# Optimization experiments

Measured on AMD Instinct MI355X. Metric: run time of the kernel, lower is better.

Reference implementation:

```python
import jax, jax.numpy as jnp
import numpy as np


def setup_inputs() -> dict:
    key = jax.random.key(0)
    k1, k2, k3, k4 = jax.random.split(key, 4)
    B, C, H, W = 4, 256, 64, 64
    Va = jax.random.normal(k1, (B, C, H, W), jnp.float32)
    Vb = jax.random.normal(k2, (B, C, H, W), jnp.float32)
    # nn.Linear(C, C, bias=False) weight, used as x @ W^T
    W_linear = jax.random.normal(k3, (C, C), jnp.float32) * 0.05
    # nn.Conv2d(C, 1, 1, bias=False) weight, init normal_(0, 0.01)
    W_gate = jax.random.normal(k4, (C,), jnp.float32) * 0.01
    return {"Va_output": Va, "Vb_output": Vb, "W_linear": W_linear,
            "W_gate": W_gate, "input_size": 512}


def reference(Va_output, Vb_output, W_linear, W_gate, input_size):
    B, C, H, W = Vb_output.shape
    A = H * W  # all_dim
    Va_flat = Va_output.reshape(B, C, A)  # [B, C, A]
    Vb_flat = Vb_output.reshape(B, C, A)
    # linear on transposed A-major tokens: Va_t @ W_linear^T -> [B, A, C]
    Va_corr = jnp.einsum('bca,dc->bad', Va_flat, W_linear)
    # correlation matrix S = Va_corr @ Vb_flat -> [B, A, A]
    S = jnp.einsum('bac,can->ban'[:3] + 'c,c' if False else 'bac,cn', Va_corr, Vb_flat) if False else jnp.einsum('bac,bcn->ban', Va_corr, Vb_flat)
    # S_c = softmax(S, dim=1); S_r = softmax(S^T, dim=1) = softmax(S, axis=2)^T
    S_c = jax.nn.softmax(S, axis=1)
    S_r = jnp.swapaxes(jax.nn.softmax(S, axis=2), 1, 2)
    Vb_att = jnp.einsum('bca,ban->bcn', Va_flat, S_r).reshape(B, C, H, W)
    Va_att = jnp.einsum('bca,ban->bcn', Vb_flat, S_c).reshape(B, C, H, W)
    # 1x1 gate conv (C -> 1, no bias) + sigmoid
    Va_mask = jax.nn.sigmoid(jnp.einsum('bchw,c->bhw', Va_att, W_gate))[:, None]
    Vb_mask = jax.nn.sigmoid(jnp.einsum('bchw,c->bhw', Vb_att, W_gate))[:, None]
    Va_out = jnp.concatenate([Va_att * Va_mask, Va_output], axis=1)  # [B, 2C, H, W]
    Vb_out = jnp.concatenate([Vb_att * Vb_mask, Vb_output], axis=1)
    return (Va_out, Vb_out, input_size)
```

## Files before the change

### kernel.cpp

```cpp
#include <hip/hip_runtime.h>

typedef _Float16 f16;
typedef f16 f16x8 __attribute__((ext_vector_type(8)));
typedef float f32x4 __attribute__((ext_vector_type(4)));
typedef short b16x8 __attribute__((ext_vector_type(8)));
typedef unsigned short u16;
typedef u16 u16x4 __attribute__((ext_vector_type(4)));

#define MFMA_F16(a,b,c)  __builtin_amdgcn_mfma_f32_16x16x32_f16((a),(b),(c),0,0,0)
#define MFMA_BF16(a,b,c) __builtin_amdgcn_mfma_f32_16x16x32_bf16((a),(b),(c),0,0,0)

static __device__ __forceinline__ u16 bf16rn(float f) {
    unsigned u = __builtin_bit_cast(unsigned, f);
    u += 0x7FFFu + ((u >> 16) & 1u);
    return (u16)(u >> 16);
}

typedef const __attribute__((address_space(1))) unsigned int* gas_p;
typedef __attribute__((address_space(3))) unsigned int* las_p;
static __device__ __forceinline__ void gll16(const void* g, void* l) {
    __builtin_amdgcn_global_load_lds((gas_p)g, (las_p)l, 16, 0, 0);
}

static constexpr int B_ = 4, C_ = 256, A_ = 4096;
static constexpr int CA   = C_ * A_;
static constexpr int BCA  = B_ * CA;
static constexpr int OUT_T = B_ * 2 * CA;
static constexpr size_t WS_Va16 = 0;
static constexpr size_t WS_Vb16 = WS_Va16 + (size_t)BCA;
static constexpr size_t WS_VaT  = WS_Vb16 + (size_t)BCA;
static constexpr size_t WS_VbT  = WS_VaT  + (size_t)BCA;
static constexpr size_t WS_Q1   = WS_VbT  + (size_t)BCA;
static constexpr size_t WS_W16  = WS_Q1   + (size_t)BCA;
static constexpr size_t WS_HALFS = WS_W16 + (size_t)(C_ * C_);

static constexpr float M0 = 48.0f;

__global__ void coatt_convw(const float* __restrict__ W, f16* __restrict__ W16) {
    int i = blockIdx.x * 256 + threadIdx.x;
    W16[i] = (f16)W[i];
}

__global__ void coatt_transpose(const float* __restrict__ Va,
                                const float* __restrict__ Vb,
                                u16* __restrict__ ws) {
    __shared__ f16 tile[64][72];
    int z = blockIdx.z; int b = z >> 1; int which = z & 1;
    const float* src = which ? Vb : Va;
    u16* cm = ws + (which ? WS_Vb16 : WS_Va16);
    f16* am = (f16*)(ws + (which ? WS_VbT : WS_VaT));
    int a0 = blockIdx.x * 64, c0 = blockIdx.y * 64;
    int t = threadIdx.x;
    int r = t >> 2, q = t & 3;

    const float* sp = src + (size_t)(b * C_ + c0 + r) * A_ + a0 + q * 16;
    f16 h[16] __attribute__((aligned(16)));
    u16 hb[16] __attribute__((aligned(16)));
#pragma unroll
    for (int i = 0; i < 4; ++i) {
        float4 v = *(const float4*)(sp + i * 4);
        h[i*4+0] = (f16)v.x; h[i*4+1] = (f16)v.y;
        h[i*4+2] = (f16)v.z; h[i*4+3] = (f16)v.w;
        hb[i*4+0] = bf16rn(v.x); hb[i*4+1] = bf16rn(v.y);
        hb[i*4+2] = bf16rn(v.z); hb[i*4+3] = bf16rn(v.w);
    }
    u16* cp = cm + (size_t)(b * C_ + c0 + r) * A_ + a0 + q * 16;
    *(u16x4*)(cp)      = *(const u16x4*)&hb[0];
    *(u16x4*)(cp + 4)  = *(const u16x4*)&hb[4];
    *(u16x4*)(cp + 8)  = *(const u16x4*)&hb[8];
    *(u16x4*)(cp + 12) = *(const u16x4*)&hb[12];
#pragma unroll
    for (int i = 0; i < 16; ++i) tile[r][q * 16 + i] = h[i];
    __syncthreads();
    f16 ht[16] __attribute__((aligned(16)));
#pragma unroll
    for (int i = 0; i < 16; ++i) ht[i] = tile[q * 16 + i][r];
    f16* ap = am + (size_t)(b * A_ + a0 + r) * C_ + c0 + q * 16;
    *(f16x8*)(ap)     = *(const f16x8*)&ht[0];
    *(f16x8*)(ap + 8) = *(const f16x8*)&ht[8];
}

__global__ __launch_bounds__(256) void coatt_q1(const f16* __restrict__ vat,
                                                const f16* __restrict__ w16,
                                                f16* __restrict__ q1) {
    int b = blockIdx.y; int a0 = blockIdx.x * 64;
    int tid = threadIdx.x, wave = tid >> 6, lane = tid & 63;
    int m = lane & 15, quad = lane >> 4;

    const f16* Ap = vat + (size_t)(b * A_ + a0 + wave * 16 + m) * C_ + quad * 8;
    f16x8 af[8];
#pragma unroll
    for (int kc = 0; kc < 8; ++kc) af[kc] = *(const f16x8*)(Ap + kc * 32);

    f32x4 acc[16];
#pragma unroll
    for (int t = 0; t < 16; ++t) acc[t] = (f32x4){0.f, 0.f, 0.f, 0.f};

#pragma unroll
    for (int kc = 0; kc < 8; ++kc) {
#pragma unroll
        for (int t = 0; t < 16; ++t) {
            f16x8 bf = *(const f16x8*)(w16 + (size_t)(t * 16 + m) * C_ + kc * 32 + quad * 8);
            acc[t] = MFMA_F16(af[kc], bf, acc[t]);
        }
    }
#pragma unroll
    for (int t = 0; t < 16; ++t) {
#pragma unroll
        for (int r = 0; r < 4; ++r) {
            int arow = a0 + wave * 16 + quad * 4 + r;
            q1[(size_t)(b * A_ + arow) * C_ + t * 16 + m] = (f16)acc[t][r];
        }
    }
}

__global__ __launch_bounds__(256, 2) void coatt_flash(const u16* __restrict__ ws,
                                                      const float* __restrict__ Wgate,
                                                      float* __restrict__ dout) {
    __shared__ __align__(16) char smem[78848];
    char* Klds = smem;
    char* Vlds = smem + 34816;
    char* Plds = smem + 69632;
    float* Olds = (float*)smem;
    float* Lsum = (float*)(smem + 69632);
    float* Gsum = (float*)(smem + 69632 + 512);

    int att = blockIdx.z, b = blockIdx.y;
    int n0 = blockIdx.x * 64;
    const f16 *Qp, *Kp; const u16* Vp; float* outp;
    if (att == 0) {
        Qp = (const f16*)(ws + WS_Q1)  + (size_t)b * CA;
        Kp = (const f16*)(ws + WS_VbT) + (size_t)b * CA;
        Vp = ws + WS_Va16 + (size_t)b * CA;
        outp = dout + (size_t)OUT_T + (size_t)b * 2 * CA;
    } else {
        Qp = (const f16*)(ws + WS_VbT) + (size_t)b * CA;
        Kp = (const f16*)(ws + WS_Q1)  + (size_t)b * CA;
        Vp = ws + WS_Vb16 + (size_t)b * CA;
        outp = dout + (size_t)b * 2 * CA;
    }

    int tid = threadIdx.x, wave = tid >> 6, lane = tid & 63;
    int i = wave >> 1, j = wave & 1;
    int m = lane & 15, quad = lane >> 4;

    f16x8 qf[2][8];
#pragma unroll
    for (int qt = 0; qt < 2; ++qt) {
        const f16* qr = Qp + (size_t)(n0 + i * 32 + qt * 16 + m) * C_ + quad * 8;
#pragma unroll
        for (int kc = 0; kc < 8; ++kc) qf[qt][kc] = *(const f16x8*)(qr + kc * 32);
    }

    f32x4 Oacc[2][8];
#pragma unroll
    for (int qt = 0; qt < 2; ++qt)
#pragma unroll
        for (int ct = 0; ct < 8; ++ct) Oacc[qt][ct] = (f32x4){0.f, 0.f, 0.f, 0.f};
    float lpart[2] = {0.f, 0.f};

    for (int kb = 0; kb < 64; ++kb) {
        int key0 = kb * 64;
        {
            const f16* kg = Kp + (size_t)(key0 + 2 * wave) * C_ + lane * 8;
            char* kl = Klds + wave * 1088;
#pragma unroll
            for (int ii = 0; ii < 8; ++ii)
                gll16(kg + ii * 2048, kl + ii * 4352);
            const u16* vg = Vp + (size_t)(wave * 8 + (lane >> 3)) * A_ + key0 + (lane & 7) * 8;
            char* vl = Vlds + wave * 1088;
#pragma unroll
            for (int ii = 0; ii < 8; ++ii)
                gll16(vg + (size_t)ii * 32 * A_, vl + ii * 4352);
        }
        __syncthreads();

        f32x4 Sc[2][2];
#pragma unroll
        for (int kt = 0; kt < 2; ++kt)
#pragma unroll
            for (int qt = 0; qt < 2; ++qt) Sc[kt][qt] = (f32x4){0.f, 0.f, 0.f, 0.f};
#pragma unroll
        for (int kc = 0; kc < 8; ++kc) {
            f16x8 kf[2];
#pragma unroll
            for (int kt = 0; kt < 2; ++kt) {
                int kl_ = j * 32 + kt * 16 + m;
                kf[kt] = *(const f16x8*)(Klds + (kl_ >> 1) * 1088 + (kl_ & 1) * 512 +
                                         kc * 64 + quad * 16);
            }
#pragma unroll
            for (int kt = 0; kt < 2; ++kt)
#pragma unroll
                for (int qt = 0; qt < 2; ++qt)
                    Sc[kt][qt] = MFMA_F16(kf[kt], qf[qt][kc], Sc[kt][qt]);
        }

#pragma unroll
        for (int qt = 0; qt < 2; ++qt) {
            int qg = i * 32 + qt * 16 + m;
#pragma unroll
            for (int kt = 0; kt < 2; ++kt) {
                u16x4 pk;
                float s4 = 0.f;
#pragma unroll
                for (int r = 0; r < 4; ++r) {
                    float p = __expf(Sc[kt][qt][r] - M0);
                    s4 += p;
                    pk[r] = bf16rn(p);
                }
                lpart[qt] += s4;
                *(u16x4*)(Plds + qg * 144 + (j * 32 + kt * 16 + quad * 4) * 2) = pk;
            }
        }
        __syncthreads();

#pragma unroll
        for (int kt = 0; kt < 2; ++kt) {
            b16x8 pf[2];
#pragma unroll
            for (int qt = 0; qt < 2; ++qt) {
                int qg = i * 32 + qt * 16 + m;
                pf[qt] = *(const b16x8*)(Plds + qg * 144 + kt * 64 + quad * 16);
            }
#pragma unroll
            for (int ct = 0; ct < 8; ++ct) {
                int c = j * 128 + ct * 16 + m;
                b16x8 vf = *(const b16x8*)(Vlds + (c >> 3) * 1088 + (c & 7) * 128 +
                                           kt * 64 + quad * 16);
#pragma unroll
                for (int qt = 0; qt < 2; ++qt)
                    Oacc[qt][ct] = MFMA_BF16(pf[qt], vf, Oacc[qt][ct]);
            }
        }
        __syncthreads();
    }

#pragma unroll
    for (int qt = 0; qt < 2; ++qt) {
        float v = lpart[qt];
        v += __shfl_xor(v, 16);
        v += __shfl_xor(v, 32);
        lpart[qt] = v;
    }
    if (lane < 16) {
#pragma unroll
        for (int qt = 0; qt < 2; ++qt)
            Lsum[j * 64 + i * 32 + qt * 16 + lane] = lpart[qt];
    }
    __syncthreads();
    float inv[2][4];
#pragma unroll
    for (int qt = 0; qt < 2; ++qt)
#pragma unroll
        for (int r = 0; r < 4; ++r) {
            int q = i * 32 + qt * 16 + quad * 4 + r;
            inv[qt][r] = 1.0f / (Lsum[q] + Lsum[64 + q]);
        }
    float gp[2][4] = {{0.f,0.f,0.f,0.f},{0.f,0.f,0.f,0.f}};
#pragma unroll
    for (int ct = 0; ct < 8; ++ct) {
        float w = Wgate[j * 128 + ct * 16 + m];
#pragma unroll
        for (int qt = 0; qt < 2; ++qt)
#pragma unroll
            for (int r = 0; r < 4; ++r) {
                float o = Oacc[qt][ct][r] * inv[qt][r];
                Oacc[qt][ct][r] = o;
                gp[qt][r] += o * w;
            }
    }
#pragma unroll
    for (int qt = 0; qt < 2; ++qt)
#pragma unroll
        for (int r = 0; r < 4; ++r) {
            float v = gp[qt][r];
            v += __shfl_xor(v, 1); v += __shfl_xor(v, 2);
            v += __shfl_xor(v, 4); v += __shfl_xor(v, 8);
            gp[qt][r] = v;
        }
    if (m == 0) {
#pragma unroll
        for (int qt = 0; qt < 2; ++qt)
#pragma unroll
            for (int r = 0; r < 4; ++r)
                Gsum[j * 64 + i * 32 + qt * 16 + quad * 4 + r] = gp[qt][r];
    }
    __syncthreads();
#pragma unroll
    for (int qt = 0; qt < 2; ++qt)
#pragma unroll
        for (int r = 0; r < 4; ++r) {
            int q = i * 32 + qt * 16 + quad * 4 + r;
            float g = Gsum[q] + Gsum[64 + q];
            float msk = 1.0f / (1.0f + __expf(-g));
#pragma unroll
            for (int ct = 0; ct < 8; ++ct) Oacc[qt][ct][r] *= msk;
        }

    for (int hf = 0; hf < 2; ++hf) {
        __syncthreads();
        if (j == hf) {
#pragma unroll
            for (int ct = 0; ct < 8; ++ct)
#pragma unroll
                for (int qt = 0; qt < 2; ++qt)
#pragma unroll
                    for (int r = 0; r < 4; ++r)
                        Olds[(ct * 16 + m) * 68 + i * 32 + qt * 16 + quad * 4 + r] =
                            Oacc[qt][ct][r];
        }
        __syncthreads();
#pragma unroll
        for (int ii = 0; ii < 8; ++ii) {
            int ci = tid + ii * 256;
            int c = ci >> 4, ch = (ci & 15) * 4;
            float4 v = *(const float4*)(Olds + c * 68 + ch);
            *(float4*)(outp + (size_t)(hf * 128 + c) * A_ + n0 + ch) = v;
        }
    }
}

__global__ void coatt_copy(const float* __restrict__ Va, const float* __restrict__ Vb,
                           const int* __restrict__ psz, float* __restrict__ dout) {
    int base = blockIdx.x * 256 + threadIdx.x;
    const float4* va4 = (const float4*)Va;
    const float4* vb4 = (const float4*)Vb;
    float4* out4 = (float4*)dout;
#pragma unroll
    for (int i = 0; i < 4; ++i) {
        int idx = base + i * 524288;
        int t = idx >> 20;
        int r = idx & 1048575;
        int b = r >> 18;
        int rr = r & 262143;
        float4 v = t ? vb4[r] : va4[r];
        out4[(size_t)t * 2097152 + (size_t)b * 524288 + 262144 + rr] = v;
    }
    if (base == 0) dout[16777216] = (float)(*psz);
}

extern "C" void kernel_launch(void* const* d_in, const int* in_sizes, int n_in,
                              void* d_out, int out_size, void* d_ws, size_t ws_size,
                              hipStream_t stream) {
    const float* Va = (const float*)d_in[0];
    const float* Vb = (const float*)d_in[1];
    const float* Wl = (const float*)d_in[2];
    const float* Wg = (const float*)d_in[3];
    const int* psz  = (const int*)d_in[4];
    float* out = (float*)d_out;
    u16* ws = (u16*)d_ws;

    if (ws_size < WS_HALFS * sizeof(u16)) return;

    coatt_convw<<<256, 256, 0, stream>>>(Wl, (f16*)(ws + WS_W16));
    coatt_transpose<<<dim3(64, 4, 8), 256, 0, stream>>>(Va, Vb, ws);
    coatt_q1<<<dim3(64, 4), 256, 0, stream>>>((const f16*)(ws + WS_VaT),
                                              (const f16*)(ws + WS_W16),
                                              (f16*)(ws + WS_Q1));
    coatt_flash<<<dim3(64, 4, 2), 256, 0, stream>>>(ws, Wg, out);
    coatt_copy<<<2048, 256, 0, stream>>>(Va, Vb, psz, out);
}
```

Before: 287.0 us.

## Load K/V fragments directly from global memory, double-buffer P, reorder block grid

The flash kernel stops staging K and V tiles in LDS through global_load_lds and instead has each wave load its MFMA fragments straight from global memory into registers. The P buffer is double-buffered so the trailing barrier per key block can be removed. LDS shrinks from about 77 KB to 35 KB. The grid is flattened so consecutive blocks cycle through batch and attention variant, which changes how blocks spread across cache. The cost is redundant global/L2 traffic, because waves that share K or V rows each fetch them separately, plus higher register pressure from holding 16 V fragments per wave.

```diff
diff --git a/kernel.cpp b/kernel.cpp
--- a/kernel.cpp
+++ b/kernel.cpp
@@ -14,12 +14,6 @@
     unsigned u = __builtin_bit_cast(unsigned, f);
     u += 0x7FFFu + ((u >> 16) & 1u);
     return (u16)(u >> 16);
-}
-
-typedef const __attribute__((address_space(1))) unsigned int* gas_p;
-typedef __attribute__((address_space(3))) unsigned int* las_p;
-static __device__ __forceinline__ void gll16(const void* g, void* l) {
-    __builtin_amdgcn_global_load_lds((gas_p)g, (las_p)l, 16, 0, 0);
 }
 
 static constexpr int B_ = 4, C_ = 256, A_ = 4096;
@@ -117,16 +111,17 @@
 __global__ __launch_bounds__(256, 2) void coatt_flash(const u16* __restrict__ ws,
                                                       const float* __restrict__ Wgate,
                                                       float* __restrict__ dout) {
-    __shared__ __align__(16) char smem[78848];
-    char* Klds = smem;
-    char* Vlds = smem + 34816;
-    char* Plds = smem + 69632;
+    __shared__ __align__(16) char smem[35840];
+    char* Plds = smem;
+    float* Lsum = (float*)(smem + 18432);
+    float* Gsum = (float*)(smem + 18432 + 512);
     float* Olds = (float*)smem;
-    float* Lsum = (float*)(smem + 69632);
-    float* Gsum = (float*)(smem + 69632 + 512);
-
-    int att = blockIdx.z, b = blockIdx.y;
-    int n0 = blockIdx.x * 64;
+
+    int p = blockIdx.x;
+    int vc = p & 7;
+    int b = vc & 3, att = vc >> 2;
+    int n0 = (p >> 3) * 64;
+
     const f16 *Qp, *Kp; const u16* Vp; float* outp;
     if (att == 0) {
         Qp = (const f16*)(ws + WS_Q1)  + (size_t)b * CA;
@@ -159,21 +154,12 @@
         for (int ct = 0; ct < 8; ++ct) Oacc[qt][ct] = (f32x4){0.f, 0.f, 0.f, 0.f};
     float lpart[2] = {0.f, 0.f};
 
+    const f16* kg0 = Kp + (size_t)(j * 32 + m) * C_ + quad * 8;
+    const u16* vg0 = Vp + (size_t)(j * 128 + m) * A_ + quad * 8;
+
     for (int kb = 0; kb < 64; ++kb) {
         int key0 = kb * 64;
-        {
-            const f16* kg = Kp + (size_t)(key0 + 2 * wave) * C_ + lane * 8;
-            char* kl = Klds + wave * 1088;
-#pragma unroll
-            for (int ii = 0; ii < 8; ++ii)
-                gll16(kg + ii * 2048, kl + ii * 4352);
-            const u16* vg = Vp + (size_t)(wave * 8 + (lane >> 3)) * A_ + key0 + (lane & 7) * 8;
-            char* vl = Vlds + wave * 1088;
-#pragma unroll
-            for (int ii = 0; ii < 8; ++ii)
-                gll16(vg + (size_t)ii * 32 * A_, vl + ii * 4352);
-        }
-        __syncthreads();
+        char* Pbuf = Plds + (kb & 1) * 9216;
 
         f32x4 Sc[2][2];
 #pragma unroll
@@ -181,19 +167,26 @@
 #pragma unroll
             for (int qt = 0; qt < 2; ++qt) Sc[kt][qt] = (f32x4){0.f, 0.f, 0.f, 0.f};
 #pragma unroll
-        for (int kc = 0; kc < 8; ++kc) {
-            f16x8 kf[2];
-#pragma unroll
-            for (int kt = 0; kt < 2; ++kt) {
-                int kl_ = j * 32 + kt * 16 + m;
-                kf[kt] = *(const f16x8*)(Klds + (kl_ >> 1) * 1088 + (kl_ & 1) * 512 +
-                                         kc * 64 + quad * 16);
-            }
+        for (int kt = 0; kt < 2; ++kt) {
+            f16x8 kf[8];
+            const f16* kg = kg0 + (size_t)(key0 + kt * 16) * C_;
+#pragma unroll
+            for (int kc = 0; kc < 8; ++kc)
+                kf[kc] = *(const f16x8*)(kg + kc * 32);
+#pragma unroll
+            for (int kc = 0; kc < 8; ++kc)
+#pragma unroll
+                for (int qt = 0; qt < 2; ++qt)
+                    Sc[kt][qt] = MFMA_F16(kf[kc], qf[qt][kc], Sc[kt][qt]);
+        }
+
+        b16x8 vf[2][8];
+#pragma unroll
+        for (int ct = 0; ct < 8; ++ct) {
+            const u16* vg = vg0 + (size_t)(ct * 16) * A_ + key0;
 #pragma unroll
             for (int kt = 0; kt < 2; ++kt)
-#pragma unroll
-                for (int qt = 0; qt < 2; ++qt)
-                    Sc[kt][qt] = MFMA_F16(kf[kt], qf[qt][kc], Sc[kt][qt]);
+                vf[kt][ct] = *(const b16x8*)(vg + kt * 32);
         }
 
 #pragma unroll
@@ -205,12 +198,12 @@
                 float s4 = 0.f;
 #pragma unroll
                 for (int r = 0; r < 4; ++r) {
-                    float p = __expf(Sc[kt][qt][r] - M0);
-                    s4 += p;
-                    pk[r] = bf16rn(p);
+                    float pv = __expf(Sc[kt][qt][r] - M0);
+                    s4 += pv;
+                    pk[r] = bf16rn(pv);
                 }
                 lpart[qt] += s4;
-                *(u16x4*)(Plds + qg * 144 + (j * 32 + kt * 16 + quad * 4) * 2) = pk;
+                *(u16x4*)(Pbuf + qg * 144 + (j * 32 + kt * 16 + quad * 4) * 2) = pk;
             }
         }
         __syncthreads();
@@ -221,21 +214,17 @@
 #pragma unroll
             for (int qt = 0; qt < 2; ++qt) {
                 int qg = i * 32 + qt * 16 + m;
-                pf[qt] = *(const b16x8*)(Plds + qg * 144 + kt * 64 + quad * 16);
+                pf[qt] = *(const b16x8*)(Pbuf + qg * 144 + kt * 64 + quad * 16);
             }
 #pragma unroll
-            for (int ct = 0; ct < 8; ++ct) {
-                int c = j * 128 + ct * 16 + m;
-                b16x8 vf = *(const b16x8*)(Vlds + (c >> 3) * 1088 + (c & 7) * 128 +
-                                           kt * 64 + quad * 16);
+            for (int ct = 0; ct < 8; ++ct)
 #pragma unroll
                 for (int qt = 0; qt < 2; ++qt)
-                    Oacc[qt][ct] = MFMA_BF16(pf[qt], vf, Oacc[qt][ct]);
-            }
-        }
-        __syncthreads();
-    }
-
+                    Oacc[qt][ct] = MFMA_BF16(pf[qt], vf[kt][ct], Oacc[qt][ct]);
+        }
+    }
+
+    __syncthreads();
 #pragma unroll
     for (int qt = 0; qt < 2; ++qt) {
         float v = lpart[qt];
@@ -358,6 +347,6 @@
     coatt_q1<<<dim3(64, 4), 256, 0, stream>>>((const f16*)(ws + WS_VaT),
                                               (const f16*)(ws + WS_W16),
                                               (f16*)(ws + WS_Q1));
-    coatt_flash<<<dim3(64, 4, 2), 256, 0, stream>>>(ws, Wg, out);
+    coatt_flash<<<512, 256, 0, stream>>>(ws, Wg, out);
     coatt_copy<<<2048, 256, 0, stream>>>(Va, Vb, psz, out);
 }
```

Result: slower. 587.6 us (+104.8%).
